# Kernel tuning notes

Hardware: AMD Instinct MI355X
Metric: run time of the kernel (lower is better)

Reference implementation:

```python
import jax, jax.numpy as jnp
import numpy as np

B, BOND, N, ATOM, UNITS = 256, 5, 128, 64, 128


def setup_inputs() -> dict:
    key = jax.random.key(0)
    k1, k2, k3 = jax.random.split(key, 3)
    adjacency = jax.random.uniform(k1, (B, BOND, N, N), dtype=jnp.float32)
    features = jax.random.normal(k2, (B, N, ATOM), dtype=jnp.float32)
    # per-sample unique kernel: (global_batch, bond_dim, atom_dim, units)
    kernel = jax.random.normal(k3, (B, BOND, ATOM, UNITS), dtype=jnp.float32) * 0.05
    return {"adjacency": adjacency, "features": features, "kernel": kernel}


def reference(adjacency, features, kernel):
    # aggregate neighbors per bond type: [B, bond, N, atom]
    x = jnp.einsum('bemn,bnd->bemd', adjacency, features)
    # per-sample, per-bond linear transform: [B, bond, N, units]
    x = jnp.einsum('bemd,bedu->bemu', x, kernel)
    # reduce over bond types, then activation: [B, N, units]
    return jax.nn.relu(jnp.sum(x, axis=1))
```

## Files before the change

### kernel.cpp

```cpp
#include <hip/hip_runtime.h>


typedef __attribute__((ext_vector_type(8))) short s8v;
typedef __attribute__((ext_vector_type(4))) float f4v;

__device__ __forceinline__ short f2bf(float f) {
    unsigned u = __builtin_bit_cast(unsigned, f);
    u += 0x7FFFu + ((u >> 16) & 1u);
    return (short)(u >> 16);
}

__device__ __forceinline__ void lds_barrier() {
    asm volatile("s_waitcnt lgkmcnt(0)" ::: "memory");
    __builtin_amdgcn_s_barrier();
    __builtin_amdgcn_sched_barrier(0);
}

__global__ __launch_bounds__(512, 4)
void rgc_kernel(const float* __restrict__ adj,
                const float* __restrict__ feat,
                const float* __restrict__ ker,
                float* __restrict__ out)
{
    __shared__ __align__(16) short featB[16 * 512];
    __shared__ __align__(16) short kerB[2][16 * 512];
    __shared__ __align__(16) short YA[8][2 * 512];

    const int tid  = threadIdx.x;
    const int w    = tid >> 6;
    const int lane = tid & 63;
    const int c16  = lane & 15;
    const int quad = lane >> 4;
    const int g    = w >> 1;
    const int h    = w & 1;

    const int bid  = blockIdx.x;
    const int wg   = ((bid & 7) << 6) | (bid >> 3);
    const int b    = wg >> 1;
    const int half = wg & 1;
    const int rowBase = 64 * half + 16 * g;

    const float* adjB = adj  + (size_t)b * (5 * 128 * 128);
    const float* feG  = feat + (size_t)b * (128 * 64);
    const float* keG  = ker  + (size_t)b * (5 * 64 * 128);
    float*       outB = out  + (size_t)b * (128 * 128);

    f4v a0[4], a1[4];
    {
        const float* ap = adjB + (rowBase + c16) * 128 + 8 * quad;
        #pragma unroll
        for (int k16 = 0; k16 < 4; ++k16) {
            a0[k16] = *(const f4v*)(ap + 32 * k16);
            a1[k16] = *(const f4v*)(ap + 32 * k16 + 4);
        }
    }

    {
        const int fd = tid & 63;
        #pragma unroll
        for (int i = 0; i < 2; ++i) {
            const int fn0 = i * 64 + (tid >> 6) * 8;
            float fv[8];
            #pragma unroll
            for (int j = 0; j < 8; ++j)
                fv[j] = feG[(fn0 + j) * 64 + fd];
            s8v v;
            #pragma unroll
            for (int j = 0; j < 8; ++j) v[j] = f2bf(fv[j]);
            *(s8v*)&featB[((fd >> 4) * 4 + (fn0 >> 5)) * 512 + ((fn0 >> 3) & 3) * 128 + (fd & 15) * 8] = v;
        }
    }

    const int ku   = tid & 127;
    const int kd0a = (tid >> 7) * 8;
    const int kd0b = 32 + kd0a;
    const int kOffA = (ku >> 4) * 1024 + (kd0a >> 5) * 512 + ((kd0a >> 3) & 3) * 128 + (ku & 15) * 8;
    const int kOffB = (ku >> 4) * 1024 + (kd0b >> 5) * 512 + ((kd0b >> 3) & 3) * 128 + (ku & 15) * 8;
    {
        float kv[16];
        #pragma unroll
        for (int j = 0; j < 8; ++j) kv[j]     = keG[(kd0a + j) * 128 + ku];
        #pragma unroll
        for (int j = 0; j < 8; ++j) kv[8 + j] = keG[(kd0b + j) * 128 + ku];
        s8v va, vb;
        #pragma unroll
        for (int j = 0; j < 8; ++j) { va[j] = f2bf(kv[j]); vb[j] = f2bf(kv[8 + j]); }
        *(s8v*)&kerB[0][kOffA] = va;
        *(s8v*)&kerB[0][kOffB] = vb;
    }
    lds_barrier();

    f4v oacc[4] = {};

    for (int e = 0; e < 5; ++e) {
        s8v af[4];
        #pragma unroll
        for (int k16 = 0; k16 < 4; ++k16) {
            #pragma unroll
            for (int j = 0; j < 4; ++j) {
                af[k16][j]     = f2bf(a0[k16][j]);
                af[k16][4 + j] = f2bf(a1[k16][j]);
            }
        }

        float kv[16];
        if (e < 4) {
            const float* kp = keG + (e + 1) * (64 * 128);
            #pragma unroll
            for (int j = 0; j < 8; ++j) kv[j]     = kp[(kd0a + j) * 128 + ku];
            #pragma unroll
            for (int j = 0; j < 8; ++j) kv[8 + j] = kp[(kd0b + j) * 128 + ku];
            const float* ap = adjB + (e + 1) * (128 * 128) + (rowBase + c16) * 128 + 8 * quad;
            #pragma unroll
            for (int k16 = 0; k16 < 4; ++k16) {
                a0[k16] = *(const f4v*)(ap + 32 * k16);
                a1[k16] = *(const f4v*)(ap + 32 * k16 + 4);
            }
            __builtin_amdgcn_sched_barrier(0);
        }

        f4v yacc[4] = {};
        #pragma unroll
        for (int k16 = 0; k16 < 4; ++k16)
            #pragma unroll
            for (int d16 = 0; d16 < 4; ++d16) {
                s8v bf = *(const s8v*)&featB[(d16 * 4 + k16) * 512 + lane * 8];
                yacc[d16] = __builtin_amdgcn_mfma_f32_16x16x32_bf16(af[k16], bf, yacc[d16], 0, 0, 0);
            }

        #pragma unroll
        for (int d16 = 0; d16 < 4; ++d16) {
            const int base = (d16 >> 1) * 512 + ((2 * d16 + (c16 >> 3)) & 3) * 128 + (c16 & 7);
            #pragma unroll
            for (int r = 0; r < 4; ++r)
                YA[w][base + (4 * quad + r) * 8] = f2bf(yacc[d16][r]);
        }

        {
            const int buf = e & 1;
            s8v afr0 = *(const s8v*)&YA[w][lane * 8];
            s8v afr1 = *(const s8v*)&YA[w][512 + lane * 8];
            #pragma unroll
            for (int n = 0; n < 4; ++n) {
                const int u16 = 4 * h + n;
                s8v b0 = *(const s8v*)&kerB[buf][(u16 * 2 + 0) * 512 + lane * 8];
                s8v b1 = *(const s8v*)&kerB[buf][(u16 * 2 + 1) * 512 + lane * 8];
                oacc[n] = __builtin_amdgcn_mfma_f32_16x16x32_bf16(afr0, b0, oacc[n], 0, 0, 0);
                oacc[n] = __builtin_amdgcn_mfma_f32_16x16x32_bf16(afr1, b1, oacc[n], 0, 0, 0);
            }
        }

        if (e < 4) {
            s8v va, vb;
            #pragma unroll
            for (int j = 0; j < 8; ++j) { va[j] = f2bf(kv[j]); vb[j] = f2bf(kv[8 + j]); }
            *(s8v*)&kerB[(e + 1) & 1][kOffA] = va;
            *(s8v*)&kerB[(e + 1) & 1][kOffB] = vb;
            lds_barrier();
        }
    }

    #pragma unroll
    for (int n = 0; n < 4; ++n)
        #pragma unroll
        for (int r = 0; r < 4; ++r)
            outB[(rowBase + 4 * quad + r) * 128 + 16 * (4 * h + n) + c16] = fmaxf(oacc[n][r], 0.f);
}

extern "C" void kernel_launch(void* const* d_in, const int* in_sizes, int n_in,
                              void* d_out, int out_size, void* d_ws, size_t ws_size,
                              hipStream_t stream)
{
    const float* adj  = (const float*)d_in[0];
    const float* feat = (const float*)d_in[1];
    const float* ker  = (const float*)d_in[2];
    rgc_kernel<<<512, 512, 0, stream>>>(adj, feat, ker, (float*)d_out);
}
```

Measured before the change: 178.3 us.

## Process one batch per block and stream adjacency via global_load_lds

New measurement: 168.8 us. 1.06x faster.

```diff
diff --git a/kernel.cpp b/kernel.cpp
--- a/kernel.cpp
+++ b/kernel.cpp
@@ -16,117 +16,119 @@
     __builtin_amdgcn_sched_barrier(0);
 }
 
-__global__ __launch_bounds__(512, 4)
+typedef __attribute__((address_space(1))) const void gas_void;
+typedef __attribute__((address_space(3))) void las_void;
+__device__ __forceinline__ void gl_lds16(const float* g, float* l) {
+#if __has_builtin(__builtin_amdgcn_global_load_lds)
+    __builtin_amdgcn_global_load_lds((gas_void*)g, (las_void*)l, 16, 0, 0);
+#else
+    const int lane = threadIdx.x & 63;
+    *(f4v*)(l + 4 * lane) = *(const f4v*)(g);
+#endif
+}
+
+__global__ __launch_bounds__(512, 2)
 void rgc_kernel(const float* __restrict__ adj,
                 const float* __restrict__ feat,
                 const float* __restrict__ ker,
                 float* __restrict__ out)
 {
+    __shared__ __align__(16) float adjF[8][4][512];
+    __shared__ __align__(16) short kerF[2][16 * 512];
     __shared__ __align__(16) short featB[16 * 512];
-    __shared__ __align__(16) short kerB[2][16 * 512];
-    __shared__ __align__(16) short YA[8][2 * 512];
+    __shared__ __align__(16) short YA[8][1024];
 
     const int tid  = threadIdx.x;
     const int w    = tid >> 6;
     const int lane = tid & 63;
     const int c16  = lane & 15;
     const int quad = lane >> 4;
-    const int g    = w >> 1;
-    const int h    = w & 1;
 
-    const int bid  = blockIdx.x;
-    const int wg   = ((bid & 7) << 6) | (bid >> 3);
-    const int b    = wg >> 1;
-    const int half = wg & 1;
-    const int rowBase = 64 * half + 16 * g;
-
+    const int b = blockIdx.x;
     const float* adjB = adj  + (size_t)b * (5 * 128 * 128);
     const float* feG  = feat + (size_t)b * (128 * 64);
     const float* keG  = ker  + (size_t)b * (5 * 64 * 128);
     float*       outB = out  + (size_t)b * (128 * 128);
 
-    f4v a0[4], a1[4];
-    {
-        const float* ap = adjB + (rowBase + c16) * 128 + 8 * quad;
+    const float* aRow = adjB + (16 * w + c16) * 128 + 8 * quad;
+
+    const int fd = tid & 63;
+    float fv[16];
+    #pragma unroll
+    for (int i = 0; i < 2; ++i)
         #pragma unroll
-        for (int k16 = 0; k16 < 4; ++k16) {
-            a0[k16] = *(const f4v*)(ap + 32 * k16);
-            a1[k16] = *(const f4v*)(ap + 32 * k16 + 4);
-        }
-    }
-
-    {
-        const int fd = tid & 63;
-        #pragma unroll
-        for (int i = 0; i < 2; ++i) {
-            const int fn0 = i * 64 + (tid >> 6) * 8;
-            float fv[8];
-            #pragma unroll
-            for (int j = 0; j < 8; ++j)
-                fv[j] = feG[(fn0 + j) * 64 + fd];
-            s8v v;
-            #pragma unroll
-            for (int j = 0; j < 8; ++j) v[j] = f2bf(fv[j]);
-            *(s8v*)&featB[((fd >> 4) * 4 + (fn0 >> 5)) * 512 + ((fn0 >> 3) & 3) * 128 + (fd & 15) * 8] = v;
-        }
-    }
+        for (int j = 0; j < 8; ++j)
+            fv[i * 8 + j] = feG[(i * 64 + (tid >> 6) * 8 + j) * 64 + fd];
 
     const int ku   = tid & 127;
     const int kd0a = (tid >> 7) * 8;
     const int kd0b = 32 + kd0a;
     const int kOffA = (ku >> 4) * 1024 + (kd0a >> 5) * 512 + ((kd0a >> 3) & 3) * 128 + (ku & 15) * 8;
     const int kOffB = (ku >> 4) * 1024 + (kd0b >> 5) * 512 + ((kd0b >> 3) & 3) * 128 + (ku & 15) * 8;
+    float kva[8], kvb[8];
+    #pragma unroll
+    for (int j = 0; j < 8; ++j) { kva[j] = keG[(kd0a + j) * 128 + ku]; kvb[j] = keG[(kd0b + j) * 128 + ku]; }
+
+    #pragma unroll
+    for (int k16 = 0; k16 < 4; ++k16) {
+        gl_lds16(aRow + 32 * k16,     &adjF[w][k16][0]);
+        gl_lds16(aRow + 32 * k16 + 4, &adjF[w][k16][256]);
+    }
+    __builtin_amdgcn_sched_barrier(0);
+
+    #pragma unroll
+    for (int i = 0; i < 2; ++i) {
+        const int fn0 = i * 64 + (tid >> 6) * 8;
+        s8v v;
+        #pragma unroll
+        for (int j = 0; j < 8; ++j) v[j] = f2bf(fv[i * 8 + j]);
+        *(s8v*)&featB[((fd >> 4) * 4 + (fn0 >> 5)) * 512 + ((fn0 >> 3) & 3) * 128 + (fd & 15) * 8] = v;
+    }
     {
-        float kv[16];
-        #pragma unroll
-        for (int j = 0; j < 8; ++j) kv[j]     = keG[(kd0a + j) * 128 + ku];
-        #pragma unroll
-        for (int j = 0; j < 8; ++j) kv[8 + j] = keG[(kd0b + j) * 128 + ku];
         s8v va, vb;
         #pragma unroll
-        for (int j = 0; j < 8; ++j) { va[j] = f2bf(kv[j]); vb[j] = f2bf(kv[8 + j]); }
-        *(s8v*)&kerB[0][kOffA] = va;
-        *(s8v*)&kerB[0][kOffB] = vb;
+        for (int j = 0; j < 8; ++j) { va[j] = f2bf(kva[j]); vb[j] = f2bf(kvb[j]); }
+        *(s8v*)&kerF[0][kOffA] = va;
+        *(s8v*)&kerF[0][kOffB] = vb;
     }
     lds_barrier();
 
-    f4v oacc[4] = {};
+    f4v oacc[8] = {};
 
     for (int e = 0; e < 5; ++e) {
-        s8v af[4];
-        #pragma unroll
-        for (int k16 = 0; k16 < 4; ++k16) {
-            #pragma unroll
-            for (int j = 0; j < 4; ++j) {
-                af[k16][j]     = f2bf(a0[k16][j]);
-                af[k16][4 + j] = f2bf(a1[k16][j]);
-            }
-        }
-
-        float kv[16];
+        float nka[8], nkb[8];
         if (e < 4) {
             const float* kp = keG + (e + 1) * (64 * 128);
             #pragma unroll
-            for (int j = 0; j < 8; ++j) kv[j]     = kp[(kd0a + j) * 128 + ku];
-            #pragma unroll
-            for (int j = 0; j < 8; ++j) kv[8 + j] = kp[(kd0b + j) * 128 + ku];
-            const float* ap = adjB + (e + 1) * (128 * 128) + (rowBase + c16) * 128 + 8 * quad;
-            #pragma unroll
-            for (int k16 = 0; k16 < 4; ++k16) {
-                a0[k16] = *(const f4v*)(ap + 32 * k16);
-                a1[k16] = *(const f4v*)(ap + 32 * k16 + 4);
-            }
+            for (int j = 0; j < 8; ++j) { nka[j] = kp[(kd0a + j) * 128 + ku]; nkb[j] = kp[(kd0b + j) * 128 + ku]; }
             __builtin_amdgcn_sched_barrier(0);
         }
 
         f4v yacc[4] = {};
         #pragma unroll
-        for (int k16 = 0; k16 < 4; ++k16)
+        for (int k16 = 0; k16 < 4; ++k16) {
+            if (e < 4) asm volatile("s_waitcnt vmcnt(22)" ::: "memory");
+            else       asm volatile("s_waitcnt vmcnt(0)"  ::: "memory");
+            __builtin_amdgcn_sched_barrier(0);
+            const f4v x0 = *(const f4v*)&adjF[w][k16][lane * 4];
+            const f4v x1 = *(const f4v*)&adjF[w][k16][256 + lane * 4];
+            asm volatile("s_waitcnt lgkmcnt(0)" ::: "memory");
+            __builtin_amdgcn_sched_barrier(0);
+            if (e < 4) {
+                const float* src = aRow + (e + 1) * 16384 + 32 * k16;
+                gl_lds16(src,     &adjF[w][k16][0]);
+                gl_lds16(src + 4, &adjF[w][k16][256]);
+            }
+            __builtin_amdgcn_sched_barrier(0);
+            s8v af;
+            #pragma unroll
+            for (int j = 0; j < 4; ++j) { af[j] = f2bf(x0[j]); af[4 + j] = f2bf(x1[j]); }
             #pragma unroll
             for (int d16 = 0; d16 < 4; ++d16) {
                 s8v bf = *(const s8v*)&featB[(d16 * 4 + k16) * 512 + lane * 8];
-                yacc[d16] = __builtin_amdgcn_mfma_f32_16x16x32_bf16(af[k16], bf, yacc[d16], 0, 0, 0);
+                yacc[d16] = __builtin_amdgcn_mfma_f32_16x16x32_bf16(af, bf, yacc[d16], 0, 0, 0);
             }
+        }
 
         #pragma unroll
         for (int d16 = 0; d16 < 4; ++d16) {
@@ -137,34 +139,32 @@
         }
 
         {
-            const int buf = e & 1;
             s8v afr0 = *(const s8v*)&YA[w][lane * 8];
             s8v afr1 = *(const s8v*)&YA[w][512 + lane * 8];
             #pragma unroll
-            for (int n = 0; n < 4; ++n) {
-                const int u16 = 4 * h + n;
-                s8v b0 = *(const s8v*)&kerB[buf][(u16 * 2 + 0) * 512 + lane * 8];
-                s8v b1 = *(const s8v*)&kerB[buf][(u16 * 2 + 1) * 512 + lane * 8];
-                oacc[n] = __builtin_amdgcn_mfma_f32_16x16x32_bf16(afr0, b0, oacc[n], 0, 0, 0);
-                oacc[n] = __builtin_amdgcn_mfma_f32_16x16x32_bf16(afr1, b1, oacc[n], 0, 0, 0);
+            for (int u16 = 0; u16 < 8; ++u16) {
+                s8v b0 = *(const s8v*)&kerF[e & 1][(u16 * 2 + 0) * 512 + lane * 8];
+                s8v b1 = *(const s8v*)&kerF[e & 1][(u16 * 2 + 1) * 512 + lane * 8];
+                oacc[u16] = __builtin_amdgcn_mfma_f32_16x16x32_bf16(afr0, b0, oacc[u16], 0, 0, 0);
+                oacc[u16] = __builtin_amdgcn_mfma_f32_16x16x32_bf16(afr1, b1, oacc[u16], 0, 0, 0);
             }
         }
 
         if (e < 4) {
             s8v va, vb;
             #pragma unroll
-            for (int j = 0; j < 8; ++j) { va[j] = f2bf(kv[j]); vb[j] = f2bf(kv[8 + j]); }
-            *(s8v*)&kerB[(e + 1) & 1][kOffA] = va;
-            *(s8v*)&kerB[(e + 1) & 1][kOffB] = vb;
+            for (int j = 0; j < 8; ++j) { va[j] = f2bf(nka[j]); vb[j] = f2bf(nkb[j]); }
+            *(s8v*)&kerF[(e + 1) & 1][kOffA] = va;
+            *(s8v*)&kerF[(e + 1) & 1][kOffB] = vb;
             lds_barrier();
         }
     }
 
     #pragma unroll
-    for (int n = 0; n < 4; ++n)
+    for (int u16 = 0; u16 < 8; ++u16)
         #pragma unroll
         for (int r = 0; r < 4; ++r)
-            outB[(rowBase + 4 * quad + r) * 128 + 16 * (4 * h + n) + c16] = fmaxf(oacc[n][r], 0.f);
+            outB[(16 * w + 4 * quad + r) * 128 + 16 * u16 + c16] = fmaxf(oacc[u16][r], 0.f);
 }
 
 extern "C" void kernel_launch(void* const* d_in, const int* in_sizes, int n_in,
@@ -174,5 +174,5 @@
     const float* adj  = (const float*)d_in[0];
     const float* feat = (const float*)d_in[1];
     const float* ker  = (const float*)d_in[2];
-    rgc_kernel<<<512, 512, 0, stream>>>(adj, feat, ker, (float*)d_out);
+    rgc_kernel<<<256, 512, 0, stream>>>(adj, feat, ker, (float*)d_out);
 }
```
